# Kernel tuning notes

Measured on AMD Instinct MI355X. Metric: run time of the kernel, lower is better.

Reference implementation:

```python
import jax, jax.numpy as jnp
import numpy as np


def log_g(x):
    # faithful to torch: where(x>=0, log(relu(x)+0.5), 5 - softplus(-x))
    return jnp.where(x >= 0, jnp.log(jax.nn.relu(x) + 0.5), 5.0 - jax.nn.softplus(-x))


def setup_inputs() -> dict:
    key = jax.random.key(0)
    ks = jax.random.split(key, 6)
    B, T, D, H = 8, 4096, 1024, 1024
    s = 1.0 / np.sqrt(D)
    return {
        "x": jax.random.normal(ks[0], (B, T, D), jnp.float32),
        "h_0": jax.random.normal(ks[1], (B, 1, H), jnp.float32),
        "Wz_w": jax.random.normal(ks[2], (D, H), jnp.float32) * s,
        "Wz_b": jax.random.normal(ks[3], (H,), jnp.float32) * 0.1,
        "Wh_w": jax.random.normal(ks[4], (D, H), jnp.float32) * s,
        "Wh_b": jax.random.normal(ks[5], (H,), jnp.float32) * 0.1,
    }


def reference(x, h_0, Wz_w, Wz_b, Wh_w, Wh_b):
    # k = W_z(x)
    k = jnp.einsum('btd,dh->bth', x, Wz_w) + Wz_b
    log_z = -jax.nn.softplus(-k)          # log sigmoid(k)
    log_coeffs = -jax.nn.softplus(k)      # log(1 - sigmoid(k))
    log_h0 = log_g(h_0)                                            # [B,1,H]
    log_tilde_h = log_g(jnp.einsum('btd,dh->bth', x, Wh_w) + Wh_b)  # [B,T,H]
    log_values = jnp.concatenate([log_h0, log_z + log_tilde_h], axis=1)  # [B,T+1,H]
    # a_star = pad(cumsum(log_coeffs, dim=1), (0,0,1,0)) -> one zero row at t=0
    a_star = jnp.pad(jnp.cumsum(log_coeffs, axis=1), ((0, 0), (1, 0), (0, 0)))  # [B,T+1,H]
    log_h = a_star + jax.lax.cumlogsumexp(log_values - a_star, axis=1)
    return jnp.exp(log_h)[:, 1:]  # [B,T,H]
```

## Files before the change

kernel.cpp:

```cpp
#include <hip/hip_runtime.h>
#include <hip/hip_bf16.h>
#include <stdint.h>

#define B_   8
#define T_   4096
#define D_   1024
#define H_   1024
#define M_   (B_ * T_)
#define NC_  64
#define TC_  64


typedef __attribute__((ext_vector_type(4))) float f32x4;
typedef __attribute__((ext_vector_type(8))) short bfr8;
typedef _Float16 f16;
typedef __attribute__((ext_vector_type(2))) _Float16 f16x2;

__device__ __forceinline__ unsigned short f2bf(float f) {
  unsigned int u = __float_as_uint(f);
  u += 0x7fffu + ((u >> 16) & 1u);
  return (unsigned short)(u >> 16);
}
__device__ __forceinline__ float bf2f(unsigned short h) {
  return __uint_as_float(((unsigned int)h) << 16);
}

__device__ __forceinline__ void gload16(const void* g, void* l) {
  __builtin_amdgcn_global_load_lds((const __attribute__((address_space(1))) void*)g,
                                   (__attribute__((address_space(3))) void*)l,
                                   16, 0, 0);
}

__device__ __forceinline__ float g_of(float hv) {
  return (hv >= 0.f) ? (hv + 0.5f)
                     : 148.4131591025766f / (1.f + __expf(-hv));
}

__global__ void prep_w(const float* __restrict__ Wz, const float* __restrict__ Wh,
                       unsigned short* __restrict__ wth, unsigned short* __restrict__ wtl,
                       float* __restrict__ whT, unsigned int* __restrict__ fcnt)
{
  if (blockIdx.x == 0 && blockIdx.y == 0 && threadIdx.x == 0) *fcnt = 0u;
  __shared__ float tile[32][33];
  int k0 = blockIdx.x * 32, n0 = blockIdx.y * 32;
  int tx = threadIdx.x & 31, ty = threadIdx.x >> 5;
  bool ish = (n0 >= 1024);
  const float* src = ish ? Wh : Wz;
  int nn0 = ish ? (n0 - 1024) : n0;
#pragma unroll
  for (int i = 0; i < 4; i++) {
    int k = k0 + ty * 4 + i;
    tile[ty * 4 + i][tx] = src[(size_t)k * 1024 + nn0 + tx];
  }
  __syncthreads();
#pragma unroll
  for (int i = 0; i < 4; i++) {
    int n = n0 + ty * 4 + i;
    float v = tile[tx][ty * 4 + i];
    unsigned short hi = f2bf(v);
    unsigned short lo = f2bf(v - bf2f(hi));
    wth[(size_t)n * 1024 + k0 + tx] = hi;
    wtl[(size_t)n * 1024 + k0 + tx] = lo;
    if (ish)
      whT[(size_t)(n - 1024) * 1024 + k0 + tx] = v;
  }
}

__global__ __launch_bounds__(256, 2) void gemm_cv(
    const float* __restrict__ x,
    const unsigned short* __restrict__ wth, const unsigned short* __restrict__ wtl,
    const float* __restrict__ bz, const float* __restrict__ bhb,
    f16x2* __restrict__ cvbuf,
    unsigned int* __restrict__ fcnt, unsigned int* __restrict__ flist,
    unsigned int fcap)
{
  __shared__ __align__(16) unsigned short As_h[4096], As_l[4096];
  __shared__ __align__(16) unsigned short Bzh[2048], Bzl[2048];
  __shared__ __align__(16) unsigned short Bhh[2048], Bhl[2048];
  int tid = threadIdx.x;
  int lane = tid & 63, wv = tid >> 6;
  int wr = wv >> 1, wc = wv & 1;
  int lrow = lane & 15, lhalf = lane >> 4;

  int bid = blockIdx.x;
  int cpx = gridDim.x >> 3;
  int swz = (bid & 7) * cpx + (bid >> 3);
  int grp = swz >> 7, wi = swz & 127;
  int mt = grp * 8 + (wi & 7);
  int nt = wi >> 3;
  int m0 = mt * 128, n0 = nt * 64;

  f32x4 accz[4][2], acch[4][2];
#pragma unroll
  for (int i = 0; i < 4; i++)
#pragma unroll
    for (int j = 0; j < 2; j++) {
      accz[i][j] = (f32x4){0.f, 0.f, 0.f, 0.f};
      acch[i][j] = (f32x4){0.f, 0.f, 0.f, 0.f};
    }

  int art = tid >> 3, ac4 = (tid & 7) * 4;
  int srow = tid >> 2, skb = (tid & 3) * 8;
  int blds = wv * 512;

  for (int k0 = 0; k0 < D_; k0 += 32) {
#pragma unroll
    for (int p = 0; p < 4; p++) {
      int row = p * 32 + art;
      uint4 vu = *(const uint4*)&x[(size_t)(m0 + row) * D_ + k0 + ac4];
      unsigned int hi01 = __builtin_amdgcn_perm(vu.y, vu.x, 0x07060302u);
      unsigned int hi23 = __builtin_amdgcn_perm(vu.w, vu.z, 0x07060302u);
      float l0 = __uint_as_float(vu.x) - __uint_as_float(vu.x & 0xffff0000u);
      float l1 = __uint_as_float(vu.y) - __uint_as_float(vu.y & 0xffff0000u);
      float l2 = __uint_as_float(vu.z) - __uint_as_float(vu.z & 0xffff0000u);
      float l3 = __uint_as_float(vu.w) - __uint_as_float(vu.w & 0xffff0000u);
      unsigned int lo01 = __builtin_amdgcn_perm(__float_as_uint(l1),
                                                __float_as_uint(l0), 0x07060302u);
      unsigned int lo23 = __builtin_amdgcn_perm(__float_as_uint(l3),
                                                __float_as_uint(l2), 0x07060302u);
      *(uint2*)&As_h[row * 32 + ac4] = make_uint2(hi01, hi23);
      *(uint2*)&As_l[row * 32 + ac4] = make_uint2(lo01, lo23);
    }
    {
      size_t gz = (size_t)(n0 + srow) * D_ + k0 + skb;
      size_t gh = (size_t)(1024 + n0 + srow) * D_ + k0 + skb;
      gload16(wth + gz, &Bzh[blds]);
      gload16(wtl + gz, &Bzl[blds]);
      gload16(wth + gh, &Bhh[blds]);
      gload16(wtl + gh, &Bhl[blds]);
    }
    __syncthreads();

    bfr8 ah[4], al[4], bzh[2], bzl[2], bhh[2], bhl[2];
    int ab = (wr * 64 + lrow) * 32 + lhalf * 8;
    int bb = (wc * 32 + lrow) * 32 + lhalf * 8;
#pragma unroll
    for (int f = 0; f < 4; f++) {
      ah[f] = *(const bfr8*)&As_h[ab + f * 512];
      al[f] = *(const bfr8*)&As_l[ab + f * 512];
    }
#pragma unroll
    for (int j = 0; j < 2; j++) {
      bzh[j] = *(const bfr8*)&Bzh[bb + j * 512];
      bzl[j] = *(const bfr8*)&Bzl[bb + j * 512];
      bhh[j] = *(const bfr8*)&Bhh[bb + j * 512];
      bhl[j] = *(const bfr8*)&Bhl[bb + j * 512];
    }
#pragma unroll
    for (int i = 0; i < 4; i++)
#pragma unroll
      for (int j = 0; j < 2; j++) {
        accz[i][j] = __builtin_amdgcn_mfma_f32_16x16x32_bf16(ah[i], bzh[j], accz[i][j], 0, 0, 0);
        accz[i][j] = __builtin_amdgcn_mfma_f32_16x16x32_bf16(al[i], bzh[j], accz[i][j], 0, 0, 0);
        accz[i][j] = __builtin_amdgcn_mfma_f32_16x16x32_bf16(ah[i], bzl[j], accz[i][j], 0, 0, 0);
        acch[i][j] = __builtin_amdgcn_mfma_f32_16x16x32_bf16(ah[i], bhh[j], acch[i][j], 0, 0, 0);
        acch[i][j] = __builtin_amdgcn_mfma_f32_16x16x32_bf16(al[i], bhh[j], acch[i][j], 0, 0, 0);
        acch[i][j] = __builtin_amdgcn_mfma_f32_16x16x32_bf16(ah[i], bhl[j], acch[i][j], 0, 0, 0);
      }
    __syncthreads();
  }

#pragma unroll
  for (int j = 0; j < 2; j++) {
    int col = n0 + wc * 32 + j * 16 + lrow;
    float kb = bz[col], hb = bhb[col];
#pragma unroll
    for (int i = 0; i < 4; i++) {
      int row0 = m0 + wr * 64 + i * 16 + lhalf * 4;
#pragma unroll
      for (int r = 0; r < 4; r++) {
        float kv = accz[i][j][r] + kb;
        float hv = acch[i][j][r] + hb;
        f16 kf = (f16)kv;
        float c  = 1.f / (1.f + __expf((float)kf));
        float v  = (1.f - c) * g_of(hv);
        size_t off = (size_t)(row0 + r) * H_ + col;
        f16x2 pr; pr[0] = kf; pr[1] = (f16)v;
        cvbuf[off] = pr;
        if (__builtin_fabsf(hv) < 1e-3f) {
          unsigned int p = atomicAdd(fcnt, 1u);
          if (p < fcap) flist[p] = (unsigned int)off;
        }
      }
    }
  }
}

__global__ void fixup_kc512(const float* __restrict__ x, const float* __restrict__ whT,
                            const float* __restrict__ bhb, f16x2* cvbuf,
                            const unsigned int* __restrict__ fcnt,
                            const unsigned int* __restrict__ flist, unsigned int fcap)
{
  unsigned int n = *fcnt; if (n > fcap) n = fcap;
  unsigned int gtid = blockIdx.x * blockDim.x + threadIdx.x;
  unsigned int nt = gridDim.x * blockDim.x;
  const unsigned int lim = (unsigned int)M_ * (unsigned int)H_;
  for (unsigned int i = gtid; i < n; i += nt) {
    unsigned int o = flist[i];
    if (o >= lim) continue;
    unsigned int row = o >> 10, col = o & 1023u;
    const float* xr = x + (size_t)row * D_;
    const float* wr = whT + (size_t)col * D_;
    float a1 = 0.f, a2 = 0.f;
    for (int d = 0; d < 512; d++)
      a1 = fmaf(xr[d], wr[d], a1);
    for (int d = 512; d < 1024; d++)
      a2 = fmaf(xr[d], wr[d], a2);
    float hs = (a1 + a2) + bhb[col];
    float g  = (hs >= 0.f) ? (hs + 0.5f)
                           : 148.4131591025766f / (1.f + __expf(-hs));
    f16x2 pr = cvbuf[o];
    float z  = 1.f / (1.f + __expf(-(float)pr[0]));
    pr[1] = (f16)(z * g);
    cvbuf[o] = pr;
  }
}

__global__ void scan_p1(const f16x2* __restrict__ cv,
                        float* __restrict__ Cc, float* __restrict__ Vv)
{
  int h = blockIdx.x * 256 + threadIdx.x;
  int ch = blockIdx.y, b = blockIdx.z;
  size_t base = ((size_t)b * T_ + (size_t)ch * TC_) * H_ + h;
  float C = 1.f, V = 0.f;
#pragma unroll 4
  for (int i = 0; i < TC_; i++) {
    f16x2 p = cv[base + (size_t)i * H_];
    float c = 1.f / (1.f + __expf((float)p[0]));
    V = fmaf(c, V, (float)p[1]);
    C *= c;
  }
  size_t o = ((size_t)b * NC_ + ch) * H_ + h;
  Cc[o] = C; Vv[o] = V;
}

__global__ void scan_p2(const float* __restrict__ h0, const float* __restrict__ Cc,
                        const float* __restrict__ Vv, float* __restrict__ Hi)
{
  int idx = blockIdx.x * 256 + threadIdx.x;
  float hs = g_of(h0[idx]);
  int b = idx >> 10, h = idx & 1023;
  for (int ch = 0; ch < NC_; ch++) {
    size_t o = ((size_t)b * NC_ + ch) * H_ + h;
    Hi[o] = hs;
    hs = fmaf(Cc[o], hs, Vv[o]);
  }
}

__global__ void scan_p3(void* buf, const float* __restrict__ Hi)
{
  __shared__ f16x2 S[TC_][256];
  const f16x2* cv = (const f16x2*)buf;
  float* out = (float*)buf;
  int t = threadIdx.x;
  int hg = blockIdx.x, ch = blockIdx.y, b = blockIdx.z;
  int col = hg * 256 + t;
  size_t base = ((size_t)b * T_ + (size_t)ch * TC_) * H_ + col;
#pragma unroll 4
  for (int r = 0; r < TC_; r++)
    S[r][t] = cv[base + (size_t)r * H_];
  __syncthreads();
  float hs = Hi[((size_t)b * NC_ + ch) * H_ + col];
#pragma unroll 4
  for (int r = 0; r < TC_; r++) {
    f16x2 p = S[r][t];
    float c = 1.f / (1.f + __expf((float)p[0]));
    hs = fmaf(c, hs, (float)p[1]);
    out[base + (size_t)r * H_] = hs;
  }
}

extern "C" void kernel_launch(void* const* d_in, const int* in_sizes, int n_in,
                              void* d_out, int out_size, void* d_ws, size_t ws_size,
                              hipStream_t stream)
{
  const float* x  = (const float*)d_in[0];
  const float* h0 = (const float*)d_in[1];
  const float* Wz = (const float*)d_in[2];
  const float* bz = (const float*)d_in[3];
  const float* Wh = (const float*)d_in[4];
  const float* bh = (const float*)d_in[5];
  char* ws = (char*)d_ws;

  const size_t MiB = 1024u * 1024u;
  unsigned int* fcnt  = (unsigned int*)(ws);
  unsigned int* flist = (unsigned int*)(ws + 4096);
  const unsigned int fcap = 250u * 1024u;
  unsigned short* wth = (unsigned short*)(ws + 2 * MiB);
  unsigned short* wtl = (unsigned short*)(ws + 6 * MiB);
  float* Cc = (float*)(ws + 10 * MiB);
  float* Vv = (float*)(ws + 12 * MiB);
  float* Hi = (float*)(ws + 14 * MiB);
  float* whT = (float*)(ws + 16 * MiB);

  f16x2* cvbuf = (f16x2*)d_out;

  prep_w<<<dim3(32, 64), 256, 0, stream>>>(Wz, Wh, wth, wtl, whT, fcnt);
  gemm_cv<<<4096, 256, 0, stream>>>(x, wth, wtl, bz, bh, cvbuf, fcnt, flist, fcap);
  fixup_kc512<<<512, 256, 0, stream>>>(x, whT, bh, cvbuf, fcnt, flist, fcap);
  scan_p1<<<dim3(4, 64, 8), 256, 0, stream>>>(cvbuf, Cc, Vv);
  scan_p2<<<32, 256, 0, stream>>>(h0, Cc, Vv, Hi);
  scan_p3<<<dim3(4, 64, 8), 256, 0, stream>>>(d_out, Hi);
}
```

Before: 667.1 us.

## Double-buffer GEMM LDS with prefetch, XOR-swizzled layout and pre-tiled weights

Rewrites the split-bf16 GEMM main loop to double-buffer its LDS tiles. The next K-tile of x is prefetched into registers and the weights are staged asynchronously while the current tile's MFMAs run, leaving one barrier per step. The hi and lo parts of A and B are interleaved in a single XOR-swizzled 64-wide row layout to avoid LDS bank conflicts. The weight prep kernel now writes the weights pre-tiled so each tile loads contiguously. The double buffers raise LDS use per block, which may reduce occupancy under launch_bounds(256,2).

```diff
diff --git a/kernel.cpp b/kernel.cpp
--- a/kernel.cpp
+++ b/kernel.cpp
@@ -36,51 +36,71 @@
                      : 148.4131591025766f / (1.f + __expf(-hv));
 }
 
-__global__ void prep_w(const float* __restrict__ Wz, const float* __restrict__ Wh,
-                       unsigned short* __restrict__ wth, unsigned short* __restrict__ wtl,
-                       float* __restrict__ whT, unsigned int* __restrict__ fcnt)
-{
-  if (blockIdx.x == 0 && blockIdx.y == 0 && threadIdx.x == 0) *fcnt = 0u;
-  __shared__ float tile[32][33];
-  int k0 = blockIdx.x * 32, n0 = blockIdx.y * 32;
-  int tx = threadIdx.x & 31, ty = threadIdx.x >> 5;
-  bool ish = (n0 >= 1024);
-  const float* src = ish ? Wh : Wz;
-  int nn0 = ish ? (n0 - 1024) : n0;
-#pragma unroll
-  for (int i = 0; i < 4; i++) {
-    int k = k0 + ty * 4 + i;
-    tile[ty * 4 + i][tx] = src[(size_t)k * 1024 + nn0 + tx];
+__global__ void prep_w2(const float* __restrict__ Wz, const float* __restrict__ Wh,
+                        unsigned short* __restrict__ wtp, float* __restrict__ whT,
+                        unsigned int* __restrict__ fcnt)
+{
+  int kt = blockIdx.x;
+  int nt = blockIdx.y;
+  int m  = blockIdx.z;
+  if (kt == 0 && nt == 0 && m == 0 && threadIdx.x == 0) *fcnt = 0u;
+  __shared__ float tile[32][65];
+  const float* W = m ? Wh : Wz;
+  int n0 = nt * 64, k0 = kt * 32;
+  int t = threadIdx.x;
+  {
+    int r = t >> 3, c0 = (t & 7) * 8;
+    const float* src = &W[(size_t)(k0 + r) * 1024 + n0 + c0];
+#pragma unroll
+    for (int i = 0; i < 8; i++) tile[r][c0 + i] = src[i];
   }
   __syncthreads();
-#pragma unroll
-  for (int i = 0; i < 4; i++) {
-    int n = n0 + ty * 4 + i;
-    float v = tile[tx][ty * 4 + i];
-    unsigned short hi = f2bf(v);
-    unsigned short lo = f2bf(v - bf2f(hi));
-    wth[(size_t)n * 1024 + k0 + tx] = hi;
-    wtl[(size_t)n * 1024 + k0 + tx] = lo;
-    if (ish)
-      whT[(size_t)(n - 1024) * 1024 + k0 + tx] = v;
+  unsigned short* out = wtp + ((size_t)(m * 16 + nt) * 32 + kt) * 4096;
+  {
+    int n = t >> 2;
+    int cb = (t & 3) * 2;
+    unsigned int u[8];
+#pragma unroll
+    for (int q = 0; q < 8; q++) {
+      unsigned short w2[2];
+#pragma unroll
+      for (int h = 0; h < 2; h++) {
+        int e = q * 2 + h;
+        int c = cb + (e >> 3), el = e & 7;
+        int s = c ^ (n & 7);
+        float v = tile[(s & 3) * 8 + el][n];
+        unsigned short hi = f2bf(v);
+        w2[h] = (s < 4) ? hi : f2bf(v - bf2f(hi));
+      }
+      u[q] = (unsigned int)w2[0] | ((unsigned int)w2[1] << 16);
+    }
+    uint4* dst = (uint4*)&out[(size_t)n * 64 + cb * 8];
+    dst[0] = make_uint4(u[0], u[1], u[2], u[3]);
+    dst[1] = make_uint4(u[4], u[5], u[6], u[7]);
+  }
+  if (m == 1) {
+    int n = t >> 2, kk0 = (t & 3) * 8;
+    float* dstf = &whT[(size_t)(n0 + n) * 1024 + k0 + kk0];
+#pragma unroll
+    for (int i = 0; i < 8; i++) dstf[i] = tile[kk0 + i][n];
   }
 }
 
 __global__ __launch_bounds__(256, 2) void gemm_cv(
     const float* __restrict__ x,
-    const unsigned short* __restrict__ wth, const unsigned short* __restrict__ wtl,
+    const unsigned short* __restrict__ wtp,
     const float* __restrict__ bz, const float* __restrict__ bhb,
     f16x2* __restrict__ cvbuf,
     unsigned int* __restrict__ fcnt, unsigned int* __restrict__ flist,
     unsigned int fcap)
 {
-  __shared__ __align__(16) unsigned short As_h[4096], As_l[4096];
-  __shared__ __align__(16) unsigned short Bzh[2048], Bzl[2048];
-  __shared__ __align__(16) unsigned short Bhh[2048], Bhl[2048];
+  __shared__ __align__(16) unsigned short Ac[2][8192];
+  __shared__ __align__(16) unsigned short Bzs[2][4096];
+  __shared__ __align__(16) unsigned short Bhs[2][4096];
   int tid = threadIdx.x;
   int lane = tid & 63, wv = tid >> 6;
   int wr = wv >> 1, wc = wv & 1;
-  int lrow = lane & 15, lhalf = lane >> 4;
+  int lrow = lane & 15, lq = lane >> 4;
 
   int bid = blockIdx.x;
   int cpx = gridDim.x >> 3;
@@ -100,14 +120,34 @@
     }
 
   int art = tid >> 3, ac4 = (tid & 7) * 4;
-  int srow = tid >> 2, skb = (tid & 3) * 8;
-  int blds = wv * 512;
-
-  for (int k0 = 0; k0 < D_; k0 += 32) {
+  int awb = art * 64 + ((((ac4 >> 3) ^ (art & 7)) << 3) | (ac4 & 4));
+  const float* xp = x + (size_t)(m0 + art) * D_ + ac4;
+
+  int fch = (lq ^ (lrow & 7)) << 3;
+  int aoff = (wr * 64 + lrow) * 64 + fch;
+  int boff = (wc * 32 + lrow) * 64 + fch;
+
+  const unsigned short* bsz = wtp + (size_t)nt * 131072 + tid * 8;
+  const unsigned short* bsh = bsz + 2097152;
+
+  uint4 xa[4];
+
+  auto loadX = [&](int kt) {
+#pragma unroll
+    for (int p = 0; p < 4; p++)
+      xa[p] = *(const uint4*)(xp + (size_t)p * 32 * D_ + kt * 32);
+  };
+  auto stageB = [&](int kt, int b) {
+#pragma unroll
+    for (int j = 0; j < 2; j++) {
+      gload16(bsz + (size_t)kt * 4096 + j * 2048, &Bzs[b][j * 2048 + tid * 8]);
+      gload16(bsh + (size_t)kt * 4096 + j * 2048, &Bhs[b][j * 2048 + tid * 8]);
+    }
+  };
+  auto writeA = [&](int b) {
 #pragma unroll
     for (int p = 0; p < 4; p++) {
-      int row = p * 32 + art;
-      uint4 vu = *(const uint4*)&x[(size_t)(m0 + row) * D_ + k0 + ac4];
+      uint4 vu = xa[p];
       unsigned int hi01 = __builtin_amdgcn_perm(vu.y, vu.x, 0x07060302u);
       unsigned int hi23 = __builtin_amdgcn_perm(vu.w, vu.z, 0x07060302u);
       float l0 = __uint_as_float(vu.x) - __uint_as_float(vu.x & 0xffff0000u);
@@ -118,47 +158,58 @@
                                                 __float_as_uint(l0), 0x07060302u);
       unsigned int lo23 = __builtin_amdgcn_perm(__float_as_uint(l3),
                                                 __float_as_uint(l2), 0x07060302u);
-      *(uint2*)&As_h[row * 32 + ac4] = make_uint2(hi01, hi23);
-      *(uint2*)&As_l[row * 32 + ac4] = make_uint2(lo01, lo23);
-    }
-    {
-      size_t gz = (size_t)(n0 + srow) * D_ + k0 + skb;
-      size_t gh = (size_t)(1024 + n0 + srow) * D_ + k0 + skb;
-      gload16(wth + gz, &Bzh[blds]);
-      gload16(wtl + gz, &Bzl[blds]);
-      gload16(wth + gh, &Bhh[blds]);
-      gload16(wtl + gh, &Bhl[blds]);
-    }
+      int bi = p * 2048 + awb;
+      *(uint2*)&Ac[b][bi]      = make_uint2(hi01, hi23);
+      *(uint2*)&Ac[b][bi ^ 32] = make_uint2(lo01, lo23);
+    }
+  };
+  auto doMFMA = [&](int cur) {
+    bfr8 ah[4], al[4], bzhv[2], bzlv[2], bhhv[2], bhlv[2];
+#pragma unroll
+    for (int f = 0; f < 4; f++) {
+      ah[f] = *(const bfr8*)&Ac[cur][aoff + f * 1024];
+      al[f] = *(const bfr8*)&Ac[cur][(aoff + f * 1024) ^ 32];
+    }
+#pragma unroll
+    for (int j = 0; j < 2; j++) {
+      bzhv[j] = *(const bfr8*)&Bzs[cur][boff + j * 1024];
+      bzlv[j] = *(const bfr8*)&Bzs[cur][(boff + j * 1024) ^ 32];
+      bhhv[j] = *(const bfr8*)&Bhs[cur][boff + j * 1024];
+      bhlv[j] = *(const bfr8*)&Bhs[cur][(boff + j * 1024) ^ 32];
+    }
+#pragma unroll
+    for (int i = 0; i < 4; i++)
+#pragma unroll
+      for (int j = 0; j < 2; j++) {
+        accz[i][j] = __builtin_amdgcn_mfma_f32_16x16x32_bf16(ah[i], bzhv[j], accz[i][j], 0, 0, 0);
+        accz[i][j] = __builtin_amdgcn_mfma_f32_16x16x32_bf16(al[i], bzhv[j], accz[i][j], 0, 0, 0);
+        accz[i][j] = __builtin_amdgcn_mfma_f32_16x16x32_bf16(ah[i], bzlv[j], accz[i][j], 0, 0, 0);
+        acch[i][j] = __builtin_amdgcn_mfma_f32_16x16x32_bf16(ah[i], bhhv[j], acch[i][j], 0, 0, 0);
+        acch[i][j] = __builtin_amdgcn_mfma_f32_16x16x32_bf16(al[i], bhhv[j], acch[i][j], 0, 0, 0);
+        acch[i][j] = __builtin_amdgcn_mfma_f32_16x16x32_bf16(ah[i], bhlv[j], acch[i][j], 0, 0, 0);
+      }
+  };
+
+  loadX(0);
+  stageB(0, 0);
+  writeA(0);
+  __syncthreads();
+
+  auto step = [&](int kt, int cur, int nxt) {
+    loadX(kt + 1);
+    stageB(kt + 1, nxt);
+    doMFMA(cur);
+    writeA(nxt);
     __syncthreads();
-
-    bfr8 ah[4], al[4], bzh[2], bzl[2], bhh[2], bhl[2];
-    int ab = (wr * 64 + lrow) * 32 + lhalf * 8;
-    int bb = (wc * 32 + lrow) * 32 + lhalf * 8;
-#pragma unroll
-    for (int f = 0; f < 4; f++) {
-      ah[f] = *(const bfr8*)&As_h[ab + f * 512];
-      al[f] = *(const bfr8*)&As_l[ab + f * 512];
-    }
-#pragma unroll
-    for (int j = 0; j < 2; j++) {
-      bzh[j] = *(const bfr8*)&Bzh[bb + j * 512];
-      bzl[j] = *(const bfr8*)&Bzl[bb + j * 512];
-      bhh[j] = *(const bfr8*)&Bhh[bb + j * 512];
-      bhl[j] = *(const bfr8*)&Bhl[bb + j * 512];
-    }
-#pragma unroll
-    for (int i = 0; i < 4; i++)
-#pragma unroll
-      for (int j = 0; j < 2; j++) {
-        accz[i][j] = __builtin_amdgcn_mfma_f32_16x16x32_bf16(ah[i], bzh[j], accz[i][j], 0, 0, 0);
-        accz[i][j] = __builtin_amdgcn_mfma_f32_16x16x32_bf16(al[i], bzh[j], accz[i][j], 0, 0, 0);
-        accz[i][j] = __builtin_amdgcn_mfma_f32_16x16x32_bf16(ah[i], bzl[j], accz[i][j], 0, 0, 0);
-        acch[i][j] = __builtin_amdgcn_mfma_f32_16x16x32_bf16(ah[i], bhh[j], acch[i][j], 0, 0, 0);
-        acch[i][j] = __builtin_amdgcn_mfma_f32_16x16x32_bf16(al[i], bhh[j], acch[i][j], 0, 0, 0);
-        acch[i][j] = __builtin_amdgcn_mfma_f32_16x16x32_bf16(ah[i], bhl[j], acch[i][j], 0, 0, 0);
-      }
-    __syncthreads();
-  }
+  };
+
+#pragma unroll 1
+  for (int kt = 0; kt < 30; kt += 2) {
+    step(kt, 0, 1);
+    step(kt + 1, 1, 0);
+  }
+  step(30, 0, 1);
+  doMFMA(1);
 
 #pragma unroll
   for (int j = 0; j < 2; j++) {
@@ -166,7 +217,7 @@
     float kb = bz[col], hb = bhb[col];
 #pragma unroll
     for (int i = 0; i < 4; i++) {
-      int row0 = m0 + wr * 64 + i * 16 + lhalf * 4;
+      int row0 = m0 + wr * 64 + i * 16 + lq * 4;
 #pragma unroll
       for (int r = 0; r < 4; r++) {
         float kv = accz[i][j][r] + kb;
@@ -286,8 +337,7 @@
   unsigned int* fcnt  = (unsigned int*)(ws);
   unsigned int* flist = (unsigned int*)(ws + 4096);
   const unsigned int fcap = 250u * 1024u;
-  unsigned short* wth = (unsigned short*)(ws + 2 * MiB);
-  unsigned short* wtl = (unsigned short*)(ws + 6 * MiB);
+  unsigned short* wtp = (unsigned short*)(ws + 2 * MiB);
   float* Cc = (float*)(ws + 10 * MiB);
   float* Vv = (float*)(ws + 12 * MiB);
   float* Hi = (float*)(ws + 14 * MiB);
@@ -295,8 +345,8 @@
 
   f16x2* cvbuf = (f16x2*)d_out;
 
-  prep_w<<<dim3(32, 64), 256, 0, stream>>>(Wz, Wh, wth, wtl, whT, fcnt);
-  gemm_cv<<<4096, 256, 0, stream>>>(x, wth, wtl, bz, bh, cvbuf, fcnt, flist, fcap);
+  prep_w2<<<dim3(32, 16, 2), 256, 0, stream>>>(Wz, Wh, wtp, whT, fcnt);
+  gemm_cv<<<4096, 256, 0, stream>>>(x, wtp, bz, bh, cvbuf, fcnt, flist, fcap);
   fixup_kc512<<<512, 256, 0, stream>>>(x, whT, bh, cvbuf, fcnt, flist, fcap);
   scan_p1<<<dim3(4, 64, 8), 256, 0, stream>>>(cvbuf, Cc, Vv);
   scan_p2<<<32, 256, 0, stream>>>(h0, Cc, Vv, Hi);
```

Result: slower. 708.0 us (+6.1%).

## Fuse chunk-summary scan pass into GEMM epilogue, recompute only flagged chunks

Applied to the files above, without the earlier changes.

The GEMM epilogue now computes each 64-row chunk's carry (product of coefficients and accumulated value) with a per-lane serial combine followed by cross-lane shuffles, then writes Cc/Vv directly. The separate scan_p1 pass over the whole cv buffer is replaced by a small kernel that recomputes summaries only for chunks containing entries the fixup kernel corrected. This removes a full read of the intermediate buffer, at the cost of more epilogue work and register pressure in the GEMM. Flagged chunks may be recomputed redundantly, once per flagged entry.

```diff
diff --git a/kernel.cpp b/kernel.cpp
--- a/kernel.cpp
+++ b/kernel.cpp
@@ -72,7 +72,8 @@
     const float* __restrict__ bz, const float* __restrict__ bhb,
     f16x2* __restrict__ cvbuf,
     unsigned int* __restrict__ fcnt, unsigned int* __restrict__ flist,
-    unsigned int fcap)
+    unsigned int fcap,
+    float* __restrict__ Cc, float* __restrict__ Vv)
 {
   __shared__ __align__(16) unsigned short As_h[4096], As_l[4096];
   __shared__ __align__(16) unsigned short Bzh[2048], Bzl[2048];
@@ -164,9 +165,11 @@
   for (int j = 0; j < 2; j++) {
     int col = n0 + wc * 32 + j * 16 + lrow;
     float kb = bz[col], hb = bhb[col];
+    float CC = 1.f, VV = 0.f;
 #pragma unroll
     for (int i = 0; i < 4; i++) {
       int row0 = m0 + wr * 64 + i * 16 + lhalf * 4;
+      float SC = 1.f, SV = 0.f;
 #pragma unroll
       for (int r = 0; r < 4; r++) {
         float kv = accz[i][j][r] + kb;
@@ -177,11 +180,32 @@
         size_t off = (size_t)(row0 + r) * H_ + col;
         f16x2 pr; pr[0] = kf; pr[1] = (f16)v;
         cvbuf[off] = pr;
+        float vr = (float)pr[1];
+        SV = fmaf(c, SV, vr);
+        SC *= c;
         if (__builtin_fabsf(hv) < 1e-3f) {
           unsigned int p = atomicAdd(fcnt, 1u);
           if (p < fcap) flist[p] = (unsigned int)off;
         }
       }
+      float oC = __shfl_xor(SC, 16);
+      float oV = __shfl_xor(SV, 16);
+      float nC = SC * oC;
+      float nV = (lane & 16) ? fmaf(SC, oV, SV)
+                             : fmaf(oC, SV, oV);
+      oC = __shfl_xor(nC, 32);
+      oV = __shfl_xor(nV, 32);
+      float gC = nC * oC;
+      float gV = (lane & 32) ? fmaf(nC, oV, nV)
+                             : fmaf(oC, nV, oV);
+      VV = fmaf(gC, VV, gV);
+      CC *= gC;
+    }
+    if (lane < 16) {
+      int bb2 = m0 >> 12;
+      int ch  = ((m0 & 4095) >> 6) + wr;
+      size_t oo = ((size_t)bb2 * NC_ + ch) * H_ + col;
+      Cc[oo] = CC; Vv[oo] = VV;
     }
   }
 }
@@ -216,22 +240,32 @@
   }
 }
 
-__global__ void scan_p1(const f16x2* __restrict__ cv,
-                        float* __restrict__ Cc, float* __restrict__ Vv)
-{
-  int h = blockIdx.x * 256 + threadIdx.x;
-  int ch = blockIdx.y, b = blockIdx.z;
-  size_t base = ((size_t)b * T_ + (size_t)ch * TC_) * H_ + h;
-  float C = 1.f, V = 0.f;
-#pragma unroll 4
-  for (int i = 0; i < TC_; i++) {
-    f16x2 p = cv[base + (size_t)i * H_];
-    float c = 1.f / (1.f + __expf((float)p[0]));
-    V = fmaf(c, V, (float)p[1]);
-    C *= c;
-  }
-  size_t o = ((size_t)b * NC_ + ch) * H_ + h;
-  Cc[o] = C; Vv[o] = V;
+__global__ void scan_p1r(const f16x2* __restrict__ cv,
+                         const unsigned int* __restrict__ fcnt,
+                         const unsigned int* __restrict__ flist, unsigned int fcap,
+                         float* __restrict__ Cc, float* __restrict__ Vv)
+{
+  unsigned int n = *fcnt; if (n > fcap) n = fcap;
+  unsigned int gtid = blockIdx.x * blockDim.x + threadIdx.x;
+  unsigned int nt = gridDim.x * blockDim.x;
+  const unsigned int lim = (unsigned int)M_ * (unsigned int)H_;
+  for (unsigned int idx = gtid; idx < n; idx += nt) {
+    unsigned int o = flist[idx];
+    if (o >= lim) continue;
+    unsigned int row = o >> 10, col = o & 1023u;
+    unsigned int b  = row >> 12;
+    unsigned int ch = (row & 4095u) >> 6;
+    size_t base = ((size_t)b * T_ + (size_t)ch * TC_) * H_ + col;
+    float C = 1.f, V = 0.f;
+    for (int i = 0; i < TC_; i++) {
+      f16x2 p = cv[base + (size_t)i * H_];
+      float c = 1.f / (1.f + __expf((float)p[0]));
+      V = fmaf(c, V, (float)p[1]);
+      C *= c;
+    }
+    size_t oo = ((size_t)b * NC_ + ch) * H_ + col;
+    Cc[oo] = C; Vv[oo] = V;
+  }
 }
 
 __global__ void scan_p2(const float* __restrict__ h0, const float* __restrict__ Cc,
@@ -296,9 +330,9 @@
   f16x2* cvbuf = (f16x2*)d_out;
 
   prep_w<<<dim3(32, 64), 256, 0, stream>>>(Wz, Wh, wth, wtl, whT, fcnt);
-  gemm_cv<<<4096, 256, 0, stream>>>(x, wth, wtl, bz, bh, cvbuf, fcnt, flist, fcap);
+  gemm_cv<<<4096, 256, 0, stream>>>(x, wth, wtl, bz, bh, cvbuf, fcnt, flist, fcap, Cc, Vv);
   fixup_kc512<<<512, 256, 0, stream>>>(x, whT, bh, cvbuf, fcnt, flist, fcap);
-  scan_p1<<<dim3(4, 64, 8), 256, 0, stream>>>(cvbuf, Cc, Vv);
+  scan_p1r<<<256, 256, 0, stream>>>(cvbuf, fcnt, flist, fcap, Cc, Vv);
   scan_p2<<<32, 256, 0, stream>>>(h0, Cc, Vv, Hi);
   scan_p3<<<dim3(4, 64, 8), 256, 0, stream>>>(d_out, Hi);
 }
```

New measurement: 684.9 us. 1.03x slower.
